# Kernel optimization log

Hardware: AMD Instinct MI355X
Metric: run time of the kernel (lower is better)

Reference implementation:

```python
import jax, jax.numpy as jnp
import numpy as np

B, D, H = 512, 256, 512

def setup_inputs() -> dict:
    key = jax.random.key(0)
    ks = jax.random.split(key, 7)
    s = lambda fan_in: 1.0 / np.sqrt(fan_in)
    return {
        "h": jax.random.normal(ks[0], (B, D), jnp.float32),
        "W1": jax.random.normal(ks[1], (2 * D, H), jnp.float32) * s(2 * D),
        "b1": jax.random.normal(ks[2], (H,), jnp.float32) * s(2 * D),
        "W2": jax.random.normal(ks[3], (H, H), jnp.float32) * s(H),
        "b2": jax.random.normal(ks[4], (H,), jnp.float32) * s(H),
        "W3": jax.random.normal(ks[5], (H, 1), jnp.float32) * s(H),
        "b3": jax.random.normal(ks[6], (1,), jnp.float32) * s(H),
    }

def reference(h, W1, b1, W2, b2, W3, b3):
    n = h.shape[0]
    # Split W1 into halves acting on hi and hj; equivalent to cat([hi,hj]) @ W1
    yi = h @ W1[:D]            # [B, H]
    yj = h @ W1[D:]            # [B, H]
    x = jnp.tanh(yi[:, None, :] + yj[None, :, :] + b1)   # [B, B, H]
    x = jnp.tanh(x @ W2 + b2)                             # [B, B, H]
    logits = (x @ W3 + b3)[..., 0]                        # [B, B]
    eye = jnp.eye(n, dtype=logits.dtype)
    return logits * (1.0 - eye) + (-20.0) * eye
```

## Files before the change

kernel.cpp:

```cpp
#include <hip/hip_runtime.h>
#include <cstdint>


#define NB 512
#define ND 256
#define NH 512
#define C2 2.885390081777927f

typedef int i32x4 __attribute__((ext_vector_type(4)));
typedef int i32x16 __attribute__((ext_vector_type(16)));
typedef unsigned int u32;
typedef unsigned char u8;

__device__ __forceinline__ float exp2_fast(float x) {
#if __has_builtin(__builtin_amdgcn_exp2f)
  return __builtin_amdgcn_exp2f(x);
#else
  return exp2f(x);
#endif
}
__device__ __forceinline__ float rcp_fast(float x) {
#if __has_builtin(__builtin_amdgcn_rcpf)
  return __builtin_amdgcn_rcpf(x);
#else
  return 1.0f / x;
#endif
}
__device__ __forceinline__ u32 perm_b32(u32 hi, u32 lo, u32 sel) {
#if __has_builtin(__builtin_amdgcn_perm)
  return __builtin_amdgcn_perm(hi, lo, sel);
#else
  u32 r = 0;
  for (int b = 0; b < 4; ++b) {
    const u32 c = (sel >> (8 * b)) & 255;
    const u32 byte = (c < 4) ? (lo >> (8 * c)) & 255 : (c < 8) ? (hi >> (8 * (c - 4))) & 255 : 0;
    r |= byte << (8 * b);
  }
  return r;
#endif
}
__device__ __forceinline__ u32 tanh_q127_magic(float u) {
  const float r = rcp_fast(exp2_fast(u) + 1.0f);
  return __builtin_bit_cast(u32, fmaf(-254.0f, r, 12583039.0f));
}

__global__ __launch_bounds__(256) void prep_all(const float* __restrict__ h,
                                                const float* __restrict__ W1,
                                                const float* __restrict__ b1,
                                                const float* __restrict__ W2,
                                                float* __restrict__ Ai,
                                                float* __restrict__ Aj,
                                                u8* __restrict__ W2q) {
  const int t = threadIdx.x;
  const int bx = blockIdx.x;
  if (bx < 512) {
    __shared__ float hs[16][68];
    __shared__ float w1t[64][36];
    __shared__ float w1b[64][36];
    const int it = bx >> 4, nt = bx & 15;
    const int i0 = it * 16, n0 = nt * 32;
    const int nn = t & 31, ig = t >> 5;
    float accA[2] = {0.f, 0.f}, accB[2] = {0.f, 0.f};
    for (int c2 = 0; c2 < 4; ++c2) {
      __syncthreads();
      {
        const int r = t >> 4, c0 = (t & 15) * 4;
        *(float4*)&hs[r][c0] = *(const float4*)(h + (size_t)(i0 + r) * ND + c2 * 64 + c0);
      }
      {
        const int r = t >> 2, c0 = (t & 3) * 8;
        const float* st = W1 + (size_t)(c2 * 64 + r) * NH + n0 + c0;
        const float* sb = W1 + (size_t)(256 + c2 * 64 + r) * NH + n0 + c0;
        const float4 a = *(const float4*)st;
        const float4 b = *(const float4*)(st + 4);
        const float4 c = *(const float4*)sb;
        const float4 d = *(const float4*)(sb + 4);
        *(float4*)&w1t[r][c0] = a;
        *(float4*)&w1t[r][c0 + 4] = b;
        *(float4*)&w1b[r][c0] = c;
        *(float4*)&w1b[r][c0 + 4] = d;
      }
      __syncthreads();
#pragma unroll 4
      for (int k4 = 0; k4 < 16; ++k4) {
        const float4 hv0 = *(const float4*)&hs[ig * 2 + 0][k4 * 4];
        const float4 hv1 = *(const float4*)&hs[ig * 2 + 1][k4 * 4];
        const float* h0 = (const float*)&hv0;
        const float* h1 = (const float*)&hv1;
#pragma unroll
        for (int j = 0; j < 4; ++j) {
          const float wtj = w1t[k4 * 4 + j][nn];
          const float wbj = w1b[k4 * 4 + j][nn];
          accA[0] = fmaf(h0[j], wtj, accA[0]);
          accA[1] = fmaf(h1[j], wtj, accA[1]);
          accB[0] = fmaf(h0[j], wbj, accB[0]);
          accB[1] = fmaf(h1[j], wbj, accB[1]);
        }
      }
    }
    const float b1n = b1[n0 + nn];
#pragma unroll
    for (int r = 0; r < 2; ++r) {
      Ai[(size_t)(i0 + ig * 2 + r) * NH + n0 + nn] = accA[r] * C2;
      Aj[(size_t)(i0 + ig * 2 + r) * NH + n0 + nn] = (accB[r] + b1n) * C2;
    }
  } else {
    const int g = (bx - 512) * 256 + t;
    const int lane = g & 63;
    const int nt = (g >> 6) & 15;
    const int ks = g >> 10;
    const int n = nt * 32 + (lane & 31);
    const int kb = ks * 32 + ((lane >> 5) << 4);
    u32 w[4];
#pragma unroll
    for (int q = 0; q < 4; ++q) {
      u32 acc = 0;
#pragma unroll
      for (int j = 0; j < 4; ++j) {
        const float wv = fminf(fmaxf(W2[(kb + q * 4 + j) * NH + n], -0.25f), 0.25f);
        const int qi = (int)rintf(wv * 508.0f);
        acc |= ((u32)(qi & 255)) << (8 * j);
      }
      w[q] = acc;
    }
    ((uint4*)W2q)[g] = make_uint4(w[0], w[1], w[2], w[3]);
  }
}

__global__ __launch_bounds__(512, 6) void pair_main(const float* __restrict__ Ai,
                                                    const float* __restrict__ Aj,
                                                    const u8* __restrict__ W2q,
                                                    const float* __restrict__ b2,
                                                    const float* __restrict__ W3,
                                                    const float* __restrict__ b3,
                                                    float* __restrict__ out) {
  __shared__ __align__(16) u8 xs[32 * 512];
  __shared__ float red[8][32];

  const int t = threadIdx.x;
  const int w = t >> 6;
  const int lane = t & 63;
  const int lhi = lane >> 5;
  const int llo = lane & 31;
  const int bx = blockIdx.x;
  const int i = bx >> 4;
  const int j0 = (bx & 15) * 32;

  i32x16 acc[2];
#pragma unroll
  for (int nt = 0; nt < 2; ++nt)
#pragma unroll
    for (int q = 0; q < 16; ++q) acc[nt][q] = 0;

  {
    const int row = t & 31;
    const int s0 = t >> 5;
    const float* ajr = Aj + (size_t)(j0 + row) * NH;
    const float* air = Ai + (size_t)i * NH;
#pragma unroll
    for (int uu = 0; uu < 2; ++uu) {
      const int s = s0 + uu * 16;
      const int k0 = s * 16;
      u32 wds[4];
#pragma unroll
      for (int q = 0; q < 4; ++q) {
        const float4 fa = *(const float4*)(ajr + k0 + q * 4);
        const float4 ga = *(const float4*)(air + k0 + q * 4);
        const u32 m0 = tanh_q127_magic(fa.x + ga.x);
        const u32 m1 = tanh_q127_magic(fa.y + ga.y);
        const u32 m2 = tanh_q127_magic(fa.z + ga.z);
        const u32 m3 = tanh_q127_magic(fa.w + ga.w);
        const u32 p01 = perm_b32(m1, m0, 0x0C0C0400u);
        const u32 p23 = perm_b32(m3, m2, 0x0C0C0400u);
        wds[q] = perm_b32(p23, p01, 0x05040100u);
      }
      ((uint4*)xs)[s * 32 + row] = make_uint4(wds[0], wds[1], wds[2], wds[3]);
    }
  }
  __syncthreads();

  const i32x4* xsv = (const i32x4*)xs;
  const int abase = lhi * 32 + llo;
  const uint4* w2v = (const uint4*)W2q + w * 128 + lane;

  i32x4 aP0 = xsv[abase];
  i32x4 aP1 = xsv[64 + abase];
  uint4 bP00 = w2v[0], bP01 = w2v[64];
  uint4 bP10 = w2v[1024], bP11 = w2v[1024 + 64];

#pragma unroll
  for (int kk = 0; kk < 8; ++kk) {
    const int ks0 = 2 * kk;
    {
      const i32x4 a = aP0;
      const i32x4 c0 = __builtin_bit_cast(i32x4, bP00);
      const i32x4 c1 = __builtin_bit_cast(i32x4, bP01);
      if (kk < 7) {
        aP0 = xsv[(ks0 + 2) * 64 + abase];
        const uint4* wp = w2v + (ks0 + 2) * 1024;
        bP00 = wp[0];
        bP01 = wp[64];
      }
      acc[0] = __builtin_amdgcn_mfma_i32_32x32x32_i8(a, c0, acc[0], 0, 0, 0);
      acc[1] = __builtin_amdgcn_mfma_i32_32x32x32_i8(a, c1, acc[1], 0, 0, 0);
    }
    {
      const i32x4 a = aP1;
      const i32x4 c0 = __builtin_bit_cast(i32x4, bP10);
      const i32x4 c1 = __builtin_bit_cast(i32x4, bP11);
      if (kk < 7) {
        aP1 = xsv[(ks0 + 3) * 64 + abase];
        const uint4* wp = w2v + (ks0 + 3) * 1024;
        bP10 = wp[0];
        bP11 = wp[64];
      }
      acc[0] = __builtin_amdgcn_mfma_i32_32x32x32_i8(a, c0, acc[0], 0, 0, 0);
      acc[1] = __builtin_amdgcn_mfma_i32_32x32x32_i8(a, c1, acc[1], 0, 0, 0);
    }
  }

  const float SCALE = (0.25f / (127.0f * 127.0f)) * C2;
  float b2c[2], w3v[2];
#pragma unroll
  for (int ntl = 0; ntl < 2; ++ntl) {
    const int n = w * 64 + ntl * 32 + llo;
    b2c[ntl] = b2[n] * C2;
    w3v[ntl] = W3[n];
  }
  float w3s = w3v[0] + w3v[1];
#pragma unroll
  for (int off = 1; off < 32; off <<= 1) w3s += __shfl_xor(w3s, off, 64);

#pragma unroll
  for (int reg = 0; reg < 16; ++reg) {
    float sr = 0.0f;
#pragma unroll
    for (int ntl = 0; ntl < 2; ++ntl) {
      const float y = fmaf((float)acc[ntl][reg], SCALE, b2c[ntl]);
      const float r = rcp_fast(exp2_fast(y) + 1.0f);
      sr = fmaf(w3v[ntl], r, sr);
    }
#pragma unroll
    for (int off = 1; off < 32; off <<= 1) sr += __shfl_xor(sr, off, 64);
    const int row = (reg & 3) + 8 * (reg >> 2) + 4 * lhi;
    if (llo == reg) red[w][row] = fmaf(-2.0f, sr, w3s);
  }
  __syncthreads();
  if (t < 32) {
    float v = b3[0];
#pragma unroll
    for (int ww = 0; ww < 8; ++ww) v += red[ww][t];
    const int j = j0 + t;
    out[i * NB + j] = (j == i) ? -20.0f : v;
  }
}

extern "C" void kernel_launch(void* const* d_in, const int* in_sizes, int n_in,
                              void* d_out, int out_size, void* d_ws, size_t ws_size,
                              hipStream_t stream) {
  const float* h = (const float*)d_in[0];
  const float* W1 = (const float*)d_in[1];
  const float* b1 = (const float*)d_in[2];
  const float* W2 = (const float*)d_in[3];
  const float* b2 = (const float*)d_in[4];
  const float* W3 = (const float*)d_in[5];
  const float* b3 = (const float*)d_in[6];
  float* out = (float*)d_out;

  float* Ai = (float*)d_ws;
  float* Aj = Ai + NB * NH;
  u8* W2q = (u8*)(Aj + NB * NH);

  prep_all<<<576, 256, 0, stream>>>(h, W1, b1, W2, Ai, Aj, W2q);
  pair_main<<<8192, 512, 0, stream>>>(Ai, Aj, W2q, b2, W3, b3, out);
}
```

Baseline: 225.5 us.

## Split pair kernel into int8 activation staging pass and separate MFMA GEMM pass

```diff
diff --git a/kernel.cpp b/kernel.cpp
--- a/kernel.cpp
+++ b/kernel.cpp
@@ -127,14 +127,45 @@
   }
 }
 
-__global__ __launch_bounds__(512, 6) void pair_main(const float* __restrict__ Ai,
-                                                    const float* __restrict__ Aj,
-                                                    const u8* __restrict__ W2q,
-                                                    const float* __restrict__ b2,
-                                                    const float* __restrict__ W3,
-                                                    const float* __restrict__ b3,
-                                                    float* __restrict__ out) {
-  __shared__ __align__(16) u8 xs[32 * 512];
+__global__ __launch_bounds__(512, 8) void stage_xq(const float* __restrict__ Ai,
+                                                   const float* __restrict__ Aj,
+                                                   u8* __restrict__ Xq) {
+  const int t = threadIdx.x;
+  const int bx = blockIdx.x;
+  const int i = bx >> 4;
+  const int j0 = (bx & 15) * 32;
+  const int row = t & 31;
+  const int s0 = t >> 5;
+  const float* ajr = Aj + (size_t)(j0 + row) * NH;
+  const float* air = Ai + (size_t)i * NH;
+  uint4* xq = (uint4*)(Xq + (size_t)bx * 16384);
+#pragma unroll
+  for (int uu = 0; uu < 2; ++uu) {
+    const int s = s0 + uu * 16;
+    const int k0 = s * 16;
+    u32 wds[4];
+#pragma unroll
+    for (int q = 0; q < 4; ++q) {
+      const float4 fa = *(const float4*)(ajr + k0 + q * 4);
+      const float4 ga = *(const float4*)(air + k0 + q * 4);
+      const u32 m0 = tanh_q127_magic(fa.x + ga.x);
+      const u32 m1 = tanh_q127_magic(fa.y + ga.y);
+      const u32 m2 = tanh_q127_magic(fa.z + ga.z);
+      const u32 m3 = tanh_q127_magic(fa.w + ga.w);
+      const u32 p01 = perm_b32(m1, m0, 0x0C0C0400u);
+      const u32 p23 = perm_b32(m3, m2, 0x0C0C0400u);
+      wds[q] = perm_b32(p23, p01, 0x05040100u);
+    }
+    xq[s * 32 + row] = make_uint4(wds[0], wds[1], wds[2], wds[3]);
+  }
+}
+
+__global__ __launch_bounds__(512, 8) void gemm_xq(const u8* __restrict__ Xq,
+                                                  const u8* __restrict__ W2q,
+                                                  const float* __restrict__ b2,
+                                                  const float* __restrict__ W3,
+                                                  const float* __restrict__ b3,
+                                                  float* __restrict__ out) {
   __shared__ float red[8][32];
 
   const int t = threadIdx.x;
@@ -152,34 +183,7 @@
 #pragma unroll
     for (int q = 0; q < 16; ++q) acc[nt][q] = 0;
 
-  {
-    const int row = t & 31;
-    const int s0 = t >> 5;
-    const float* ajr = Aj + (size_t)(j0 + row) * NH;
-    const float* air = Ai + (size_t)i * NH;
-#pragma unroll
-    for (int uu = 0; uu < 2; ++uu) {
-      const int s = s0 + uu * 16;
-      const int k0 = s * 16;
-      u32 wds[4];
-#pragma unroll
-      for (int q = 0; q < 4; ++q) {
-        const float4 fa = *(const float4*)(ajr + k0 + q * 4);
-        const float4 ga = *(const float4*)(air + k0 + q * 4);
-        const u32 m0 = tanh_q127_magic(fa.x + ga.x);
-        const u32 m1 = tanh_q127_magic(fa.y + ga.y);
-        const u32 m2 = tanh_q127_magic(fa.z + ga.z);
-        const u32 m3 = tanh_q127_magic(fa.w + ga.w);
-        const u32 p01 = perm_b32(m1, m0, 0x0C0C0400u);
-        const u32 p23 = perm_b32(m3, m2, 0x0C0C0400u);
-        wds[q] = perm_b32(p23, p01, 0x05040100u);
-      }
-      ((uint4*)xs)[s * 32 + row] = make_uint4(wds[0], wds[1], wds[2], wds[3]);
-    }
-  }
-  __syncthreads();
-
-  const i32x4* xsv = (const i32x4*)xs;
+  const i32x4* xsv = (const i32x4*)(Xq + (size_t)bx * 16384);
   const int abase = lhi * 32 + llo;
   const uint4* w2v = (const uint4*)W2q + w * 128 + lane;
 
@@ -188,6 +192,7 @@
   uint4 bP00 = w2v[0], bP01 = w2v[64];
   uint4 bP10 = w2v[1024], bP11 = w2v[1024 + 64];
 
+  __builtin_amdgcn_s_setprio(1);
 #pragma unroll
   for (int kk = 0; kk < 8; ++kk) {
     const int ks0 = 2 * kk;
@@ -218,6 +223,135 @@
       acc[1] = __builtin_amdgcn_mfma_i32_32x32x32_i8(a, c1, acc[1], 0, 0, 0);
     }
   }
+  __builtin_amdgcn_s_setprio(0);
+
+  const float SCALE = (0.25f / (127.0f * 127.0f)) * C2;
+  float b2c[2], w3v[2];
+#pragma unroll
+  for (int ntl = 0; ntl < 2; ++ntl) {
+    const int n = w * 64 + ntl * 32 + llo;
+    b2c[ntl] = b2[n] * C2;
+    w3v[ntl] = W3[n];
+  }
+  float w3s = w3v[0] + w3v[1];
+#pragma unroll
+  for (int off = 1; off < 32; off <<= 1) w3s += __shfl_xor(w3s, off, 64);
+
+#pragma unroll
+  for (int reg = 0; reg < 16; ++reg) {
+    float sr = 0.0f;
+#pragma unroll
+    for (int ntl = 0; ntl < 2; ++ntl) {
+      const float y = fmaf((float)acc[ntl][reg], SCALE, b2c[ntl]);
+      const float r = rcp_fast(exp2_fast(y) + 1.0f);
+      sr = fmaf(w3v[ntl], r, sr);
+    }
+#pragma unroll
+    for (int off = 1; off < 32; off <<= 1) sr += __shfl_xor(sr, off, 64);
+    const int row = (reg & 3) + 8 * (reg >> 2) + 4 * lhi;
+    if (llo == reg) red[w][row] = fmaf(-2.0f, sr, w3s);
+  }
+  __syncthreads();
+  if (t < 32) {
+    float v = b3[0];
+#pragma unroll
+    for (int ww = 0; ww < 8; ++ww) v += red[ww][t];
+    const int j = j0 + t;
+    out[i * NB + j] = (j == i) ? -20.0f : v;
+  }
+}
+
+__global__ __launch_bounds__(512, 6) void pair_main(const float* __restrict__ Ai,
+                                                    const float* __restrict__ Aj,
+                                                    const u8* __restrict__ W2q,
+                                                    const float* __restrict__ b2,
+                                                    const float* __restrict__ W3,
+                                                    const float* __restrict__ b3,
+                                                    float* __restrict__ out) {
+  __shared__ __align__(16) u8 xs[32 * 512];
+  __shared__ float red[8][32];
+
+  const int t = threadIdx.x;
+  const int w = t >> 6;
+  const int lane = t & 63;
+  const int lhi = lane >> 5;
+  const int llo = lane & 31;
+  const int bx = blockIdx.x;
+  const int i = bx >> 4;
+  const int j0 = (bx & 15) * 32;
+
+  i32x16 acc[2];
+#pragma unroll
+  for (int nt = 0; nt < 2; ++nt)
+#pragma unroll
+    for (int q = 0; q < 16; ++q) acc[nt][q] = 0;
+
+  {
+    const int row = t & 31;
+    const int s0 = t >> 5;
+    const float* ajr = Aj + (size_t)(j0 + row) * NH;
+    const float* air = Ai + (size_t)i * NH;
+#pragma unroll
+    for (int uu = 0; uu < 2; ++uu) {
+      const int s = s0 + uu * 16;
+      const int k0 = s * 16;
+      u32 wds[4];
+#pragma unroll
+      for (int q = 0; q < 4; ++q) {
+        const float4 fa = *(const float4*)(ajr + k0 + q * 4);
+        const float4 ga = *(const float4*)(air + k0 + q * 4);
+        const u32 m0 = tanh_q127_magic(fa.x + ga.x);
+        const u32 m1 = tanh_q127_magic(fa.y + ga.y);
+        const u32 m2 = tanh_q127_magic(fa.z + ga.z);
+        const u32 m3 = tanh_q127_magic(fa.w + ga.w);
+        const u32 p01 = perm_b32(m1, m0, 0x0C0C0400u);
+        const u32 p23 = perm_b32(m3, m2, 0x0C0C0400u);
+        wds[q] = perm_b32(p23, p01, 0x05040100u);
+      }
+      ((uint4*)xs)[s * 32 + row] = make_uint4(wds[0], wds[1], wds[2], wds[3]);
+    }
+  }
+  __syncthreads();
+
+  const i32x4* xsv = (const i32x4*)xs;
+  const int abase = lhi * 32 + llo;
+  const uint4* w2v = (const uint4*)W2q + w * 128 + lane;
+
+  i32x4 aP0 = xsv[abase];
+  i32x4 aP1 = xsv[64 + abase];
+  uint4 bP00 = w2v[0], bP01 = w2v[64];
+  uint4 bP10 = w2v[1024], bP11 = w2v[1024 + 64];
+
+#pragma unroll
+  for (int kk = 0; kk < 8; ++kk) {
+    const int ks0 = 2 * kk;
+    {
+      const i32x4 a = aP0;
+      const i32x4 c0 = __builtin_bit_cast(i32x4, bP00);
+      const i32x4 c1 = __builtin_bit_cast(i32x4, bP01);
+      if (kk < 7) {
+        aP0 = xsv[(ks0 + 2) * 64 + abase];
+        const uint4* wp = w2v + (ks0 + 2) * 1024;
+        bP00 = wp[0];
+        bP01 = wp[64];
+      }
+      acc[0] = __builtin_amdgcn_mfma_i32_32x32x32_i8(a, c0, acc[0], 0, 0, 0);
+      acc[1] = __builtin_amdgcn_mfma_i32_32x32x32_i8(a, c1, acc[1], 0, 0, 0);
+    }
+    {
+      const i32x4 a = aP1;
+      const i32x4 c0 = __builtin_bit_cast(i32x4, bP10);
+      const i32x4 c1 = __builtin_bit_cast(i32x4, bP11);
+      if (kk < 7) {
+        aP1 = xsv[(ks0 + 3) * 64 + abase];
+        const uint4* wp = w2v + (ks0 + 3) * 1024;
+        bP10 = wp[0];
+        bP11 = wp[64];
+      }
+      acc[0] = __builtin_amdgcn_mfma_i32_32x32x32_i8(a, c0, acc[0], 0, 0, 0);
+      acc[1] = __builtin_amdgcn_mfma_i32_32x32x32_i8(a, c1, acc[1], 0, 0, 0);
+    }
+  }
 
   const float SCALE = (0.25f / (127.0f * 127.0f)) * C2;
   float b2c[2], w3v[2];
@@ -270,7 +404,17 @@
   float* Ai = (float*)d_ws;
   float* Aj = Ai + NB * NH;
   u8* W2q = (u8*)(Aj + NB * NH);
+  u8* Xq = W2q + NB * NH;
+
+  const size_t XQ_OFF = (size_t)NB * NH * 4 * 2 + (size_t)NB * NH;
+  const size_t XQ_BYTES = (size_t)8192 * 16384;
 
   prep_all<<<576, 256, 0, stream>>>(h, W1, b1, W2, Ai, Aj, W2q);
-  pair_main<<<8192, 512, 0, stream>>>(Ai, Aj, W2q, b2, W3, b3, out);
-}
+
+  if (ws_size >= XQ_OFF + XQ_BYTES) {
+    stage_xq<<<8192, 512, 0, stream>>>(Ai, Aj, Xq);
+    gemm_xq<<<8192, 512, 0, stream>>>(Xq, W2q, b2, W3, b3, out);
+  } else {
+    pair_main<<<8192, 512, 0, stream>>>(Ai, Aj, W2q, b2, W3, b3, out);
+  }
+}
```

Result: slower. 300.8 us (+33.4%).
